# Performance work log

Hardware: AMD Instinct MI355X
Metric: run time of the kernel (lower is better)

## Reference

```python
import jax, jax.numpy as jnp
import numpy as np

B, D = 8192, 256      # batch, input_dim == n_nodes
ENC = 256             # encoder_dim
DEC = 64              # decoder_dim
THR = 0.1             # adjacency threshold


def setup_inputs() -> dict:
    key = jax.random.key(0)
    ks = jax.random.split(key, 9)
    s = lambda k, sh, fan: jax.random.normal(k, sh, jnp.float32) / np.sqrt(fan).astype(np.float32)
    return {
        "x": jax.random.normal(ks[0], (B, D), jnp.float32),
        "eps": jax.random.normal(ks[1], (B, D), jnp.float32),
        "W_enc": s(ks[2], (D, ENC), D), "b_enc": jnp.zeros((ENC,), jnp.float32),
        "W_mu": s(ks[3], (ENC, D), ENC), "b_mu": jnp.zeros((D,), jnp.float32),
        "W_lv": s(ks[4], (ENC, D), ENC), "b_lv": jnp.zeros((D,), jnp.float32),
        "graph_param": jax.random.normal(ks[5], (D, D), jnp.float32),
        "W_emb": s(ks[6], (D, DEC), 1), "b_emb": jnp.zeros((D, DEC), jnp.float32),
        "W_g1": s(ks[7], (DEC, DEC // 2), DEC), "b_g1": jnp.zeros((DEC // 2,), jnp.float32),
        "W_g2": s(ks[8], (DEC // 2, 1), DEC // 2), "b_g2": jnp.zeros((1,), jnp.float32),
        "iter_": 100,
    }


def _learned_graph(graph_param, iter_):
    # LearnedGraph.forward: sigmoid, force self-loops=1, threshold after iter 50
    g = jax.nn.sigmoid(graph_param)
    eye = jnp.eye(g.shape[0], dtype=g.dtype)
    g = g * (1.0 - eye) + eye
    if iter_ > 50:  # iter_ is a static Python int
        g = jnp.where(g > THR, g, 0.0)  # nn.Threshold(THR, 0)
    return g


def _gcn_norm(adj):
    # DGL GraphConv(norm='both') with edge_weight: messages weighted by adj values,
    # but degree normalization uses structural (unweighted) edge counts.
    mask = (adj != 0).astype(adj.dtype)
    dout = jnp.maximum(mask.sum(1), 1.0)  # out-degree of src j (row sums)
    din = jnp.maximum(mask.sum(0), 1.0)   # in-degree of dst i (col sums)
    # out[i] = sum_j adj[j,i] * x[j] / sqrt(dout[j] * din[i])  ->  M[dst, src]
    return (adj / jnp.sqrt(dout)[:, None] / jnp.sqrt(din)[None, :]).T


def reference(x, eps, W_enc, b_enc, W_mu, b_mu, W_lv, b_lv,
              graph_param, W_emb, b_emb, W_g1, b_g1, W_g2, b_g2, iter_):
    # VAE encoder (Linear + ReLU, then mu/logvar heads)
    h = jax.nn.relu(x @ W_enc + b_enc)
    mu = h @ W_mu + b_mu
    logvar = h @ W_lv + b_lv
    z = mu + eps * jnp.exp(0.5 * logvar)                 # [B, D]
    # learned adjacency over the D feature-nodes
    adj = _learned_graph(graph_param, iter_)             # [D, D]
    # per-feature node embedding: Linear(1, DEC) + tanh per feature
    b_z = jnp.tanh(z[:, :, None] * W_emb[None] + b_emb[None])  # [B, D, DEC]
    # two GraphConv layers (shared adjacency per batch element)
    M = _gcn_norm(adj)                                   # [D, D]
    h1 = jax.nn.relu(jnp.einsum('ij,bjd->bid', M, b_z) @ W_g1 + b_g1)  # [B, D, 32]
    h2 = jnp.einsum('ij,bjd->bid', M, h1) @ W_g2 + b_g2                # [B, D, 1]
    x_hat = h2.reshape(B, -1)                            # [B, D]
    return x_hat, adj, mu, logvar
```

## Files before the change

kernel.cpp:

```cpp
#include <hip/hip_runtime.h>

typedef __bf16 bf16_t;
typedef __bf16 bf16x4 __attribute__((ext_vector_type(4)));
typedef __bf16 bf16x8 __attribute__((ext_vector_type(8)));
typedef float  floatx4 __attribute__((ext_vector_type(4)));
typedef unsigned long long u64;

#define MFMA16(a, b, c) __builtin_amdgcn_mfma_f32_16x16x32_bf16((a), (b), (c), 0, 0, 0)

#define ADJ_OFF  2097152
#define MU_OFF   2162688
#define LV_OFF   4259840

#define TWO_LOG2E 2.8853900817779268f

__device__ __forceinline__ float fast_tanh2(float argE2) {
    float e = __builtin_amdgcn_exp2f(argE2);
    return 1.0f - 2.0f * __builtin_amdgcn_rcpf(e + 1.0f);
}

__device__ __forceinline__ bf16x8 cvt8(const float* p) {
    const floatx4 a = *(const floatx4*)p;
    const floatx4 b = *(const floatx4*)(p + 4);
    bf16x8 r;
#pragma unroll
    for (int j = 0; j < 4; j++) { r[j] = (bf16_t)a[j]; r[4 + j] = (bf16_t)b[j]; }
    return r;
}

__global__ __launch_bounds__(256) void k_prep(
    const float* __restrict__ We, const float* __restrict__ Wm,
    const float* __restrict__ Wl, const float* __restrict__ Wemb,
    const float* __restrict__ bemb, const float* __restrict__ gp,
    const int* __restrict__ iterp, bf16_t* __restrict__ Wt,
    bf16_t* __restrict__ wepack, bf16_t* __restrict__ bepack,
    u64* __restrict__ rowbits) {
    __shared__ float tile[32][33];
    const int b = blockIdx.x, tid = threadIdx.x;
    if (b < 192) {
        const int m = b >> 6, t6 = b & 63;
        const int K0 = (t6 >> 3) << 5, N0 = (t6 & 7) << 5;
        const float* src = (m == 0) ? We : ((m == 1) ? Wm : Wl);
#pragma unroll
        for (int p = 0; p < 4; p++) {
            const int idx = p * 256 + tid;
            tile[idx >> 5][idx & 31] = src[(K0 + (idx >> 5)) * 256 + N0 + (idx & 31)];
        }
        __syncthreads();
        bf16_t* dst = Wt + m * 65536;
#pragma unroll
        for (int p = 0; p < 4; p++) {
            const int idx = p * 256 + tid;
            const int nn = idx >> 5, kk = idx & 31;
            dst[(N0 + nn) * 256 + K0 + kk] = (bf16_t)tile[kk][nn];
        }
    } else if (b < 200) {
        const int base = (b - 192) * 2048;
#pragma unroll
        for (int p = 0; p < 8; p++) {
            const int idx = base + p * 256 + tid;
            wepack[idx] = (bf16_t)(TWO_LOG2E * Wemb[idx]);
        }
    } else if (b < 208) {
        const int base = (b - 200) * 2048;
#pragma unroll
        for (int p = 0; p < 8; p++) {
            const int idx = base + p * 256 + tid;
            bepack[idx] = (bf16_t)(TWO_LOG2E * bemb[idx]);
        }
    } else {
        const int j = b - 208;
        const bool thr = (*iterp) > 50;
        float g = 1.0f / (1.0f + expf(-gp[j * 256 + tid]));
        if (tid == j) g = 1.0f;
        if (thr && !(g > 0.1f)) g = 0.0f;
        const u64 bal = __ballot(g != 0.0f);
        if ((tid & 63) == 0) rowbits[j * 4 + (tid >> 6)] = bal;
    }
}

__global__ __launch_bounds__(256) void k_mkM(
    const float* __restrict__ gp, const int* __restrict__ iterp,
    const u64* __restrict__ rowbits, bf16_t* __restrict__ Mb,
    float* __restrict__ adjOut) {
    __shared__ u64 bits[256][4];
    const int j = blockIdx.x, t = threadIdx.x;
#pragma unroll
    for (int p = 0; p < 4; p++) {
        const int idx = p * 256 + t;
        bits[idx >> 2][idx & 3] = rowbits[idx];
    }
    __syncthreads();
    const int w64 = t >> 6, sh = t & 63;
    int cnt = 0;
#pragma unroll 8
    for (int jp = 0; jp < 256; jp++)
        cnt += (int)((bits[jp][w64] >> sh) & 1ull);
    const int rc = (int)(__popcll(bits[j][0]) + __popcll(bits[j][1]) +
                         __popcll(bits[j][2]) + __popcll(bits[j][3]));
    const float rso = rsqrtf((float)(rc < 1 ? 1 : rc));
    const float rsi = rsqrtf((float)(cnt < 1 ? 1 : cnt));
    float g = 1.0f / (1.0f + expf(-gp[j * 256 + t]));
    if (t == j) g = 1.0f;
    if ((*iterp) > 50 && !(g > 0.1f)) g = 0.0f;
    if (adjOut) adjOut[j * 256 + t] = g;
    Mb[t * 256 + j] = (bf16_t)(g * rso * rsi);
}

__global__ __launch_bounds__(512) void k_ench(
    const float* __restrict__ X, const bf16_t* __restrict__ Wt,
    const float* __restrict__ benc, const float* __restrict__ bmu,
    const float* __restrict__ blv,
    float* __restrict__ MuOut, float* __restrict__ LvOut) {
    __shared__ __align__(16) bf16_t Xs[64 * 264];
    __shared__ __align__(16) bf16_t Hs[64 * 264];
    const bf16_t* Bte = Wt;
    const bf16_t* Btm = Wt + 65536;
    const bf16_t* Btl = Wt + 131072;
    const int tid = threadIdx.x;
    const int r0 = blockIdx.x * 64;
    const int w = tid >> 6;
    const int lane = tid & 63;
    const int n = lane & 15, q = lane >> 4;
    const int cw = w * 32;
    const floatx4 z4 = {0.f, 0.f, 0.f, 0.f};

#pragma unroll
    for (int p = 0; p < 4; p++) {
        const int e0 = (p * 512 + tid) * 8;
        const int row = e0 >> 8, col = e0 & 255;
        *(bf16x8*)(Xs + row * 264 + col) = cvt8(X + (r0 + row) * 256 + col);
    }
    __syncthreads();

    floatx4 ah[4][2];
#pragma unroll
    for (int rt = 0; rt < 4; rt++)
#pragma unroll
        for (int tc = 0; tc < 2; tc++) ah[rt][tc] = z4;
#pragma unroll 2
    for (int k0 = 0; k0 < 256; k0 += 32) {
        bf16x8 a[4], b[2];
#pragma unroll
        for (int rt = 0; rt < 4; rt++)
            a[rt] = *(const bf16x8*)(Xs + (rt * 16 + n) * 264 + k0 + q * 8);
#pragma unroll
        for (int tc = 0; tc < 2; tc++)
            b[tc] = *(const bf16x8*)(Bte + (cw + tc * 16 + n) * 256 + k0 + q * 8);
#pragma unroll
        for (int rt = 0; rt < 4; rt++)
#pragma unroll
            for (int tc = 0; tc < 2; tc++)
                ah[rt][tc] = MFMA16(a[rt], b[tc], ah[rt][tc]);
    }
#pragma unroll
    for (int tc = 0; tc < 2; tc++) {
        const int col = cw + tc * 16 + n;
        const float bv = benc[col];
#pragma unroll
        for (int rt = 0; rt < 4; rt++)
#pragma unroll
            for (int r = 0; r < 4; r++)
                Hs[(rt * 16 + q * 4 + r) * 264 + col] =
                    (bf16_t)fmaxf(ah[rt][tc][r] + bv, 0.0f);
    }
    __syncthreads();

    {
        floatx4 am[4][2];
#pragma unroll
        for (int rt = 0; rt < 4; rt++)
#pragma unroll
            for (int tc = 0; tc < 2; tc++) am[rt][tc] = z4;
#pragma unroll 2
        for (int k0 = 0; k0 < 256; k0 += 32) {
            bf16x8 a[4], bm_[2];
#pragma unroll
            for (int rt = 0; rt < 4; rt++)
                a[rt] = *(const bf16x8*)(Hs + (rt * 16 + n) * 264 + k0 + q * 8);
#pragma unroll
            for (int tc = 0; tc < 2; tc++)
                bm_[tc] = *(const bf16x8*)(Btm + (cw + tc * 16 + n) * 256 + k0 + q * 8);
#pragma unroll
            for (int rt = 0; rt < 4; rt++)
#pragma unroll
                for (int tc = 0; tc < 2; tc++)
                    am[rt][tc] = MFMA16(a[rt], bm_[tc], am[rt][tc]);
        }
#pragma unroll
        for (int tc = 0; tc < 2; tc++) {
            const int col = cw + tc * 16 + n;
            const float bmv = bmu[col];
#pragma unroll
            for (int rt = 0; rt < 4; rt++)
#pragma unroll
                for (int r = 0; r < 4; r++)
                    MuOut[(r0 + rt * 16 + q * 4 + r) * 256 + col] = am[rt][tc][r] + bmv;
        }
    }

    {
        floatx4 al[4][2];
#pragma unroll
        for (int rt = 0; rt < 4; rt++)
#pragma unroll
            for (int tc = 0; tc < 2; tc++) al[rt][tc] = z4;
#pragma unroll 2
        for (int k0 = 0; k0 < 256; k0 += 32) {
            bf16x8 a[4], bl_[2];
#pragma unroll
            for (int rt = 0; rt < 4; rt++)
                a[rt] = *(const bf16x8*)(Hs + (rt * 16 + n) * 264 + k0 + q * 8);
#pragma unroll
            for (int tc = 0; tc < 2; tc++)
                bl_[tc] = *(const bf16x8*)(Btl + (cw + tc * 16 + n) * 256 + k0 + q * 8);
#pragma unroll
            for (int rt = 0; rt < 4; rt++)
#pragma unroll
                for (int tc = 0; tc < 2; tc++)
                    al[rt][tc] = MFMA16(a[rt], bl_[tc], al[rt][tc]);
        }
#pragma unroll
        for (int tc = 0; tc < 2; tc++) {
            const int col = cw + tc * 16 + n;
            const float blvv = blv[col];
#pragma unroll
            for (int rt = 0; rt < 4; rt++)
#pragma unroll
                for (int r = 0; r < 4; r++)
                    LvOut[(r0 + rt * 16 + q * 4 + r) * 256 + col] = al[rt][tc][r] + blvv;
        }
    }
}

__global__ __launch_bounds__(512, 4) void k_gcn(
    const float* __restrict__ Mu, const float* __restrict__ Lv,
    const float* __restrict__ Eps, const bf16_t* __restrict__ wepack,
    const bf16_t* __restrict__ bepack, const float* __restrict__ Wg1,
    const float* __restrict__ bg1, const float* __restrict__ Wg2,
    const bf16_t* __restrict__ Mb, float* __restrict__ Vout) {
    __shared__ __align__(16) bf16_t smem[128 * 256];
    __shared__ float zs[1024];
    const int tid = threadIdx.x;
    const int lane = tid & 63;
    const int w = tid >> 6;
    const int n = lane & 15, q = lane >> 4;
    const int bg = blockIdx.x;
    const floatx4 z4 = {0.f, 0.f, 0.f, 0.f};

    {
        const int gi = bg * 1024 + tid;
        zs[tid] = fmaf(Eps[gi], __expf(0.5f * Lv[gi]), Mu[gi]);
        const int gi2 = gi + 512;
        zs[tid + 512] = fmaf(Eps[gi2], __expf(0.5f * Lv[gi2]), Mu[gi2]);
    }

    bf16x8 wg1f[2][2];
#pragma unroll
    for (int ks = 0; ks < 2; ks++)
#pragma unroll
        for (int te = 0; te < 2; te++)
#pragma unroll
            for (int j = 0; j < 8; j++)
                wg1f[ks][te][j] = (bf16_t)Wg1[(ks * 32 + q * 8 + j) * 32 + te * 16 + n];
    __syncthreads();

#pragma unroll
    for (int jt2 = 0; jt2 < 2; jt2++) {
        const int j0 = (w * 2 + jt2) * 16;
        const int jA = j0 + n;
        const bf16x8 we0 = *(const bf16x8*)(wepack + jA * 64 + q * 8);
        const bf16x8 we1 = *(const bf16x8*)(wepack + jA * 64 + 32 + q * 8);
        const bf16x8 be0 = *(const bf16x8*)(bepack + jA * 64 + q * 8);
        const bf16x8 be1 = *(const bf16x8*)(bepack + jA * 64 + 32 + q * 8);
        float wf0[8], wf1[8], bf0[8], bf1[8];
#pragma unroll
        for (int j = 0; j < 8; j++) {
            wf0[j] = (float)we0[j]; wf1[j] = (float)we1[j];
            bf0[j] = (float)be0[j]; bf1[j] = (float)be1[j];
        }
        const int j8a = (j0 >> 3) + (q >> 1);
        const int jlo = (q & 1) * 4;
        const int sw = ((j8a ^ (n & 7)) << 3) + jlo;
#pragma unroll
        for (int bl = 0; bl < 4; bl++) {
            const float zv = zs[bl * 256 + jA];
            bf16x8 a0, a1;
#pragma unroll
            for (int j = 0; j < 8; j++) {
                a0[j] = (bf16_t)fast_tanh2(fmaf(zv, wf0[j], bf0[j]));
                a1[j] = (bf16_t)fast_tanh2(fmaf(zv, wf1[j], bf1[j]));
            }
            floatx4 c0 = z4, c1 = z4;
            c0 = MFMA16(a0, wg1f[0][0], c0);
            c0 = MFMA16(a1, wg1f[1][0], c0);
            c1 = MFMA16(a0, wg1f[0][1], c1);
            c1 = MFMA16(a1, wg1f[1][1], c1);
            bf16x4 s0, s1;
#pragma unroll
            for (int r = 0; r < 4; r++) { s0[r] = (bf16_t)c0[r]; s1[r] = (bf16_t)c1[r]; }
            *(bf16x4*)(smem + (bl * 32 + n) * 256 + sw) = s0;
            *(bf16x4*)(smem + (bl * 32 + 16 + n) * 256 + sw) = s1;
        }
    }
    __syncthreads();

    const int i0 = w * 32;
    floatx4 acc[2][8];
#pragma unroll
    for (int ti = 0; ti < 2; ti++)
#pragma unroll
        for (int tc = 0; tc < 8; tc++) acc[ti][tc] = z4;
#pragma unroll
    for (int k0 = 0; k0 < 256; k0 += 32) {
        const int k8 = k0 >> 3;
        bf16x8 a[2], b[8];
#pragma unroll
        for (int ti = 0; ti < 2; ti++)
            a[ti] = *(const bf16x8*)(Mb + (i0 + ti * 16 + n) * 256 + k0 + q * 8);
#pragma unroll
        for (int tc = 0; tc < 8; tc++)
            b[tc] = *(const bf16x8*)(smem + (tc * 16 + n) * 256 +
                                     (((k8 + q) ^ (n & 7)) << 3));
        __builtin_amdgcn_s_setprio(1);
#pragma unroll
        for (int ti = 0; ti < 2; ti++)
#pragma unroll
            for (int tc = 0; tc < 8; tc++)
                acc[ti][tc] = MFMA16(a[ti], b[tc], acc[ti][tc]);
        __builtin_amdgcn_s_setprio(0);
    }

    const float w2a = Wg2[n],      w2b = Wg2[16 + n];
    const float b1a = bg1[n],      b1b = bg1[16 + n];
    float v32[32];
#pragma unroll
    for (int bl = 0; bl < 4; bl++)
#pragma unroll
        for (int ti = 0; ti < 2; ti++)
#pragma unroll
            for (int r = 0; r < 4; r++)
                v32[bl * 8 + ti * 4 + r] =
                    fmaxf(acc[ti][2 * bl][r] + b1a, 0.0f) * w2a +
                    fmaxf(acc[ti][2 * bl + 1][r] + b1b, 0.0f) * w2b;
    const bool h0 = (lane & 1), h1_ = (lane & 2), h2 = (lane & 4), h3 = (lane & 8);
    float u16[16];
#pragma unroll
    for (int p = 0; p < 16; p++) {
        const float keep = h0 ? v32[2 * p + 1] : v32[2 * p];
        const float send = h0 ? v32[2 * p] : v32[2 * p + 1];
        u16[p] = keep + __shfl_xor(send, 1, 64);
    }
    float u8[8];
#pragma unroll
    for (int p = 0; p < 8; p++) {
        const float keep = h1_ ? u16[2 * p + 1] : u16[2 * p];
        const float send = h1_ ? u16[2 * p] : u16[2 * p + 1];
        u8[p] = keep + __shfl_xor(send, 2, 64);
    }
    float u4[4];
#pragma unroll
    for (int p = 0; p < 4; p++) {
        const float keep = h2 ? u8[2 * p + 1] : u8[2 * p];
        const float send = h2 ? u8[2 * p] : u8[2 * p + 1];
        u4[p] = keep + __shfl_xor(send, 4, 64);
    }
    float u2[2];
#pragma unroll
    for (int p = 0; p < 2; p++) {
        const float keep = h3 ? u4[2 * p + 1] : u4[2 * p];
        const float send = h3 ? u4[2 * p] : u4[2 * p + 1];
        u2[p] = keep + __shfl_xor(send, 8, 64);
    }
    {
        const int i_out = i0 + ((n >> 2) & 1) * 16 + q * 4 + (n & 3);
        const int blv = n >> 3;
        Vout[bg * 1024 + blv * 256 + i_out] = u2[0];
        Vout[bg * 1024 + (2 + blv) * 256 + i_out] = u2[1];
    }
}

__global__ __launch_bounds__(512) void k_out(
    float* __restrict__ VX, const bf16_t* __restrict__ Mb,
    const float* __restrict__ bg2) {
    __shared__ __align__(16) bf16_t va[64 * 264];
    const int tid = threadIdx.x;
    const int lane = tid & 63;
    const int w = tid >> 6;
    const int n = lane & 15, q = lane >> 4;
    const int r0 = blockIdx.x * 64;

#pragma unroll
    for (int p = 0; p < 8; p++) {
        const int i4 = p * 512 + tid;
        const int row = i4 >> 6, c4 = (i4 & 63) * 4;
        const floatx4 v = *(const floatx4*)(VX + (r0 + row) * 256 + c4);
        bf16x4 s;
#pragma unroll
        for (int r = 0; r < 4; r++) s[r] = (bf16_t)v[r];
        *(bf16x4*)(va + row * 264 + c4) = s;
    }
    __syncthreads();

    const int cw = w * 32;
    const floatx4 z4 = {0.f, 0.f, 0.f, 0.f};
    floatx4 acc[4][2];
#pragma unroll
    for (int rt = 0; rt < 4; rt++)
#pragma unroll
        for (int tc = 0; tc < 2; tc++) acc[rt][tc] = z4;
#pragma unroll 2
    for (int k0 = 0; k0 < 256; k0 += 32) {
        bf16x8 a[4], b[2];
#pragma unroll
        for (int rt = 0; rt < 4; rt++)
            a[rt] = *(const bf16x8*)(va + (rt * 16 + n) * 264 + k0 + q * 8);
#pragma unroll
        for (int tc = 0; tc < 2; tc++)
            b[tc] = *(const bf16x8*)(Mb + (cw + tc * 16 + n) * 256 + k0 + q * 8);
#pragma unroll
        for (int rt = 0; rt < 4; rt++)
#pragma unroll
            for (int tc = 0; tc < 2; tc++)
                acc[rt][tc] = MFMA16(a[rt], b[tc], acc[rt][tc]);
    }
    const float bv = bg2[0];
#pragma unroll
    for (int tc = 0; tc < 2; tc++) {
        const int col = cw + tc * 16 + n;
#pragma unroll
        for (int rt = 0; rt < 4; rt++)
#pragma unroll
            for (int r = 0; r < 4; r++)
                VX[(r0 + rt * 16 + q * 4 + r) * 256 + col] = acc[rt][tc][r] + bv;
    }
}

__global__ __launch_bounds__(256) void k_adj(
    const float* __restrict__ gp, const int* __restrict__ iterp,
    float* __restrict__ adjOut) {
    const int o = blockIdx.x * 256 + threadIdx.x;
    const int j = o >> 8, i = o & 255;
    float g = 1.0f / (1.0f + expf(-gp[o]));
    if (i == j) g = 1.0f;
    if ((*iterp) > 50 && !(g > 0.1f)) g = 0.0f;
    adjOut[o] = g;
}

extern "C" void kernel_launch(void* const* d_in, const int* in_sizes, int n_in,
                              void* d_out, int out_size, void* d_ws, size_t ws_size,
                              hipStream_t stream) {
    const float* x    = (const float*)d_in[0];
    const float* eps  = (const float*)d_in[1];
    const float* Wenc = (const float*)d_in[2];
    const float* benc = (const float*)d_in[3];
    const float* Wmu  = (const float*)d_in[4];
    const float* bmu  = (const float*)d_in[5];
    const float* Wlv  = (const float*)d_in[6];
    const float* blv  = (const float*)d_in[7];
    const float* gp   = (const float*)d_in[8];
    const float* Wemb = (const float*)d_in[9];
    const float* bemb = (const float*)d_in[10];
    const float* Wg1  = (const float*)d_in[11];
    const float* bg1  = (const float*)d_in[12];
    const float* Wg2  = (const float*)d_in[13];
    const float* bg2  = (const float*)d_in[14];
    const int*   itr  = (const int*)d_in[15];
    (void)in_sizes; (void)n_in; (void)out_size;

    float* xhat = (float*)d_out;
    float* adjO = xhat + ADJ_OFF;
    float* muo  = xhat + MU_OFF;
    float* lvo  = xhat + LV_OFF;

    const bool usews = (d_ws != nullptr && ws_size >= 262144);
    char* scr = usews ? (char*)d_ws : (char*)adjO;
    bf16_t* Mb      = (bf16_t*)scr;
    bf16_t* wepack  = (bf16_t*)(scr + 131072);
    bf16_t* bepack  = (bf16_t*)(scr + 163840);
    u64*    rowbits = (u64*)(scr + 196608);
    bf16_t* Wt      = (bf16_t*)((char*)d_out + 4194304);

    k_prep<<<dim3(464), dim3(256), 0, stream>>>(Wenc, Wmu, Wlv, Wemb, bemb,
                                                gp, itr, Wt, wepack, bepack,
                                                rowbits);
    k_mkM <<<dim3(256), dim3(256), 0, stream>>>(gp, itr, rowbits, Mb,
                                                usews ? adjO : nullptr);
    k_ench<<<dim3(128), dim3(512), 0, stream>>>(x, Wt, benc, bmu, blv, muo, lvo);
    k_gcn <<<dim3(2048), dim3(512), 0, stream>>>(muo, lvo, eps, wepack, bepack,
                                                 Wg1, bg1, Wg2, Mb, xhat);
    k_out <<<dim3(128), dim3(512), 0, stream>>>(xhat, Mb, bg2);
    if (!usews)
        k_adj<<<dim3(256), dim3(256), 0, stream>>>(gp, itr, adjO);
}
```

Before: 190.9 us.

## Merge M-build into encoder kernel, prepack Wg1, halve GCN shared tile

The normalized-adjacency builder (k_mkM) is folded into the encoder kernel as extra blocks, so one launch is removed and the two independent jobs can overlap. Wg1 is converted to bf16 once in the prep kernel, which replaces a per-block strided fp32 gather in k_gcn with vector loads. k_gcn now handles the four batch rows in two halves using a 32KB instead of 64KB shared tile and fewer accumulators. This should lower LDS and register pressure and raise occupancy, at the cost of an extra barrier and of reloading the embedding weights per half.

New measurement: 221.9 us. 16.3% more time.

```diff
diff --git a/kernel.cpp b/kernel.cpp
--- a/kernel.cpp
+++ b/kernel.cpp
@@ -32,9 +32,10 @@
     const float* __restrict__ We, const float* __restrict__ Wm,
     const float* __restrict__ Wl, const float* __restrict__ Wemb,
     const float* __restrict__ bemb, const float* __restrict__ gp,
-    const int* __restrict__ iterp, bf16_t* __restrict__ Wt,
-    bf16_t* __restrict__ wepack, bf16_t* __restrict__ bepack,
-    u64* __restrict__ rowbits) {
+    const int* __restrict__ iterp, const float* __restrict__ Wg1,
+    bf16_t* __restrict__ Wt, bf16_t* __restrict__ wepack,
+    bf16_t* __restrict__ bepack, u64* __restrict__ rowbits,
+    bf16_t* __restrict__ wg1pk) {
     __shared__ float tile[32][33];
     const int b = blockIdx.x, tid = threadIdx.x;
     if (b < 192) {
@@ -68,7 +69,7 @@
             const int idx = base + p * 256 + tid;
             bepack[idx] = (bf16_t)(TWO_LOG2E * bemb[idx]);
         }
-    } else {
+    } else if (b < 464) {
         const int j = b - 208;
         const bool thr = (*iterp) > 50;
         float g = 1.0f / (1.0f + expf(-gp[j * 256 + tid]));
@@ -76,48 +77,58 @@
         if (thr && !(g > 0.1f)) g = 0.0f;
         const u64 bal = __ballot(g != 0.0f);
         if ((tid & 63) == 0) rowbits[j * 4 + (tid >> 6)] = bal;
-    }
-}
-
-__global__ __launch_bounds__(256) void k_mkM(
-    const float* __restrict__ gp, const int* __restrict__ iterp,
-    const u64* __restrict__ rowbits, bf16_t* __restrict__ Mb,
-    float* __restrict__ adjOut) {
-    __shared__ u64 bits[256][4];
-    const int j = blockIdx.x, t = threadIdx.x;
-#pragma unroll
-    for (int p = 0; p < 4; p++) {
-        const int idx = p * 256 + t;
-        bits[idx >> 2][idx & 3] = rowbits[idx];
-    }
-    __syncthreads();
-    const int w64 = t >> 6, sh = t & 63;
-    int cnt = 0;
-#pragma unroll 8
-    for (int jp = 0; jp < 256; jp++)
-        cnt += (int)((bits[jp][w64] >> sh) & 1ull);
-    const int rc = (int)(__popcll(bits[j][0]) + __popcll(bits[j][1]) +
-                         __popcll(bits[j][2]) + __popcll(bits[j][3]));
-    const float rso = rsqrtf((float)(rc < 1 ? 1 : rc));
-    const float rsi = rsqrtf((float)(cnt < 1 ? 1 : cnt));
-    float g = 1.0f / (1.0f + expf(-gp[j * 256 + t]));
-    if (t == j) g = 1.0f;
-    if ((*iterp) > 50 && !(g > 0.1f)) g = 0.0f;
-    if (adjOut) adjOut[j * 256 + t] = g;
-    Mb[t * 256 + j] = (bf16_t)(g * rso * rsi);
-}
-
-__global__ __launch_bounds__(512) void k_ench(
+    } else {
+#pragma unroll
+        for (int idx = tid; idx < 2048; idx += 256) {
+            const int jj = idx & 7, qq = (idx >> 3) & 3, nn = (idx >> 5) & 15;
+            const int te = (idx >> 9) & 1, ks = (idx >> 10) & 1;
+            wg1pk[idx] = (bf16_t)Wg1[(ks * 32 + qq * 8 + jj) * 32 + te * 16 + nn];
+        }
+    }
+}
+
+__global__ __launch_bounds__(512) void k_mid(
     const float* __restrict__ X, const bf16_t* __restrict__ Wt,
     const float* __restrict__ benc, const float* __restrict__ bmu,
-    const float* __restrict__ blv,
-    float* __restrict__ MuOut, float* __restrict__ LvOut) {
+    const float* __restrict__ blv, float* __restrict__ MuOut,
+    float* __restrict__ LvOut, const float* __restrict__ gp,
+    const int* __restrict__ iterp, const u64* __restrict__ rowbits,
+    bf16_t* __restrict__ Mb, float* __restrict__ adjOut) {
     __shared__ __align__(16) bf16_t Xs[64 * 264];
     __shared__ __align__(16) bf16_t Hs[64 * 264];
+    const int tid = threadIdx.x;
+
+    if (blockIdx.x >= 128) {
+        u64* bits = (u64*)Xs;
+        const int jb = (blockIdx.x - 128) * 2;
+#pragma unroll
+        for (int p = 0; p < 2; p++) {
+            const int idx = p * 512 + tid;
+            bits[idx] = rowbits[idx];
+        }
+        __syncthreads();
+        const int sub = tid >> 8, col = tid & 255;
+        const int j = jb + sub;
+        const int w64 = col >> 6, sh = col & 63;
+        int cnt = 0;
+#pragma unroll 8
+        for (int jp = 0; jp < 256; jp++)
+            cnt += (int)((bits[jp * 4 + w64] >> sh) & 1ull);
+        const int rc = (int)(__popcll(bits[j * 4 + 0]) + __popcll(bits[j * 4 + 1]) +
+                             __popcll(bits[j * 4 + 2]) + __popcll(bits[j * 4 + 3]));
+        const float rso = rsqrtf((float)(rc < 1 ? 1 : rc));
+        const float rsi = rsqrtf((float)(cnt < 1 ? 1 : cnt));
+        float g = 1.0f / (1.0f + expf(-gp[j * 256 + col]));
+        if (col == j) g = 1.0f;
+        if ((*iterp) > 50 && !(g > 0.1f)) g = 0.0f;
+        if (adjOut) adjOut[j * 256 + col] = g;
+        Mb[col * 256 + j] = (bf16_t)(g * rso * rsi);
+        return;
+    }
+
     const bf16_t* Bte = Wt;
     const bf16_t* Btm = Wt + 65536;
     const bf16_t* Btl = Wt + 131072;
-    const int tid = threadIdx.x;
     const int r0 = blockIdx.x * 64;
     const int w = tid >> 6;
     const int lane = tid & 63;
@@ -236,10 +247,10 @@
 __global__ __launch_bounds__(512, 4) void k_gcn(
     const float* __restrict__ Mu, const float* __restrict__ Lv,
     const float* __restrict__ Eps, const bf16_t* __restrict__ wepack,
-    const bf16_t* __restrict__ bepack, const float* __restrict__ Wg1,
+    const bf16_t* __restrict__ bepack, const bf16_t* __restrict__ wg1pk,
     const float* __restrict__ bg1, const float* __restrict__ Wg2,
     const bf16_t* __restrict__ Mb, float* __restrict__ Vout) {
-    __shared__ __align__(16) bf16_t smem[128 * 256];
+    __shared__ __align__(16) bf16_t smem[64 * 256];
     __shared__ float zs[1024];
     const int tid = threadIdx.x;
     const int lane = tid & 63;
@@ -254,129 +265,123 @@
         const int gi2 = gi + 512;
         zs[tid + 512] = fmaf(Eps[gi2], __expf(0.5f * Lv[gi2]), Mu[gi2]);
     }
-
-    bf16x8 wg1f[2][2];
-#pragma unroll
-    for (int ks = 0; ks < 2; ks++)
-#pragma unroll
-        for (int te = 0; te < 2; te++)
-#pragma unroll
-            for (int j = 0; j < 8; j++)
-                wg1f[ks][te][j] = (bf16_t)Wg1[(ks * 32 + q * 8 + j) * 32 + te * 16 + n];
     __syncthreads();
 
-#pragma unroll
-    for (int jt2 = 0; jt2 < 2; jt2++) {
-        const int j0 = (w * 2 + jt2) * 16;
-        const int jA = j0 + n;
-        const bf16x8 we0 = *(const bf16x8*)(wepack + jA * 64 + q * 8);
-        const bf16x8 we1 = *(const bf16x8*)(wepack + jA * 64 + 32 + q * 8);
-        const bf16x8 be0 = *(const bf16x8*)(bepack + jA * 64 + q * 8);
-        const bf16x8 be1 = *(const bf16x8*)(bepack + jA * 64 + 32 + q * 8);
-        float wf0[8], wf1[8], bf0[8], bf1[8];
-#pragma unroll
-        for (int j = 0; j < 8; j++) {
-            wf0[j] = (float)we0[j]; wf1[j] = (float)we1[j];
-            bf0[j] = (float)be0[j]; bf1[j] = (float)be1[j];
-        }
-        const int j8a = (j0 >> 3) + (q >> 1);
-        const int jlo = (q & 1) * 4;
-        const int sw = ((j8a ^ (n & 7)) << 3) + jlo;
-#pragma unroll
-        for (int bl = 0; bl < 4; bl++) {
-            const float zv = zs[bl * 256 + jA];
-            bf16x8 a0, a1;
-#pragma unroll
-            for (int j = 0; j < 8; j++) {
-                a0[j] = (bf16_t)fast_tanh2(fmaf(zv, wf0[j], bf0[j]));
-                a1[j] = (bf16_t)fast_tanh2(fmaf(zv, wf1[j], bf1[j]));
+    const float w2a = Wg2[n],  w2b = Wg2[16 + n];
+    const float b1a = bg1[n],  b1b = bg1[16 + n];
+    const int i0 = w * 32;
+    const bool h0 = (lane & 1), h1_ = (lane & 2), h2 = (lane & 4), h3 = (lane & 8);
+
+#pragma unroll
+    for (int half = 0; half < 2; half++) {
+        bf16x8 wg1f[2][2];
+#pragma unroll
+        for (int ks = 0; ks < 2; ks++)
+#pragma unroll
+            for (int te = 0; te < 2; te++)
+                wg1f[ks][te] = *(const bf16x8*)(wg1pk +
+                    ((ks * 2 + te) * 16 + n) * 32 + q * 8);
+
+#pragma unroll
+        for (int jt2 = 0; jt2 < 2; jt2++) {
+            const int j0 = (w * 2 + jt2) * 16;
+            const int jA = j0 + n;
+            const bf16x8 we0 = *(const bf16x8*)(wepack + jA * 64 + q * 8);
+            const bf16x8 we1 = *(const bf16x8*)(wepack + jA * 64 + 32 + q * 8);
+            const bf16x8 be0 = *(const bf16x8*)(bepack + jA * 64 + q * 8);
+            const bf16x8 be1 = *(const bf16x8*)(bepack + jA * 64 + 32 + q * 8);
+            const int j8a = (j0 >> 3) + (q >> 1);
+            const int jlo = (q & 1) * 4;
+            const int sw = ((j8a ^ (n & 7)) << 3) + jlo;
+#pragma unroll
+            for (int blh = 0; blh < 2; blh++) {
+                const float zv = zs[(half * 2 + blh) * 256 + jA];
+                bf16x8 a0, a1;
+#pragma unroll
+                for (int j = 0; j < 8; j++) {
+                    a0[j] = (bf16_t)fast_tanh2(fmaf(zv, (float)we0[j], (float)be0[j]));
+                    a1[j] = (bf16_t)fast_tanh2(fmaf(zv, (float)we1[j], (float)be1[j]));
+                }
+                floatx4 c0 = z4, c1 = z4;
+                c0 = MFMA16(a0, wg1f[0][0], c0);
+                c0 = MFMA16(a1, wg1f[1][0], c0);
+                c1 = MFMA16(a0, wg1f[0][1], c1);
+                c1 = MFMA16(a1, wg1f[1][1], c1);
+                bf16x4 s0, s1;
+#pragma unroll
+                for (int r = 0; r < 4; r++) { s0[r] = (bf16_t)c0[r]; s1[r] = (bf16_t)c1[r]; }
+                *(bf16x4*)(smem + (blh * 32 + n) * 256 + sw) = s0;
+                *(bf16x4*)(smem + (blh * 32 + 16 + n) * 256 + sw) = s1;
             }
-            floatx4 c0 = z4, c1 = z4;
-            c0 = MFMA16(a0, wg1f[0][0], c0);
-            c0 = MFMA16(a1, wg1f[1][0], c0);
-            c1 = MFMA16(a0, wg1f[0][1], c1);
-            c1 = MFMA16(a1, wg1f[1][1], c1);
-            bf16x4 s0, s1;
-#pragma unroll
-            for (int r = 0; r < 4; r++) { s0[r] = (bf16_t)c0[r]; s1[r] = (bf16_t)c1[r]; }
-            *(bf16x4*)(smem + (bl * 32 + n) * 256 + sw) = s0;
-            *(bf16x4*)(smem + (bl * 32 + 16 + n) * 256 + sw) = s1;
-        }
-    }
-    __syncthreads();
-
-    const int i0 = w * 32;
-    floatx4 acc[2][8];
-#pragma unroll
-    for (int ti = 0; ti < 2; ti++)
-#pragma unroll
-        for (int tc = 0; tc < 8; tc++) acc[ti][tc] = z4;
-#pragma unroll
-    for (int k0 = 0; k0 < 256; k0 += 32) {
-        const int k8 = k0 >> 3;
-        bf16x8 a[2], b[8];
+        }
+        __syncthreads();
+
+        floatx4 acc[2][4];
 #pragma unroll
         for (int ti = 0; ti < 2; ti++)
-            a[ti] = *(const bf16x8*)(Mb + (i0 + ti * 16 + n) * 256 + k0 + q * 8);
-#pragma unroll
-        for (int tc = 0; tc < 8; tc++)
-            b[tc] = *(const bf16x8*)(smem + (tc * 16 + n) * 256 +
-                                     (((k8 + q) ^ (n & 7)) << 3));
-        __builtin_amdgcn_s_setprio(1);
+#pragma unroll
+            for (int tc = 0; tc < 4; tc++) acc[ti][tc] = z4;
+#pragma unroll
+        for (int k0 = 0; k0 < 256; k0 += 32) {
+            const int k8 = k0 >> 3;
+            bf16x8 a[2], b[4];
+#pragma unroll
+            for (int ti = 0; ti < 2; ti++)
+                a[ti] = *(const bf16x8*)(Mb + (i0 + ti * 16 + n) * 256 + k0 + q * 8);
+#pragma unroll
+            for (int tc = 0; tc < 4; tc++)
+                b[tc] = *(const bf16x8*)(smem + (tc * 16 + n) * 256 +
+                                         (((k8 + q) ^ (n & 7)) << 3));
+            __builtin_amdgcn_s_setprio(1);
+#pragma unroll
+            for (int ti = 0; ti < 2; ti++)
+#pragma unroll
+                for (int tc = 0; tc < 4; tc++)
+                    acc[ti][tc] = MFMA16(a[ti], b[tc], acc[ti][tc]);
+            __builtin_amdgcn_s_setprio(0);
+        }
+
+        float v16[16];
 #pragma unroll
         for (int ti = 0; ti < 2; ti++)
 #pragma unroll
-            for (int tc = 0; tc < 8; tc++)
-                acc[ti][tc] = MFMA16(a[ti], b[tc], acc[ti][tc]);
-        __builtin_amdgcn_s_setprio(0);
-    }
-
-    const float w2a = Wg2[n],      w2b = Wg2[16 + n];
-    const float b1a = bg1[n],      b1b = bg1[16 + n];
-    float v32[32];
-#pragma unroll
-    for (int bl = 0; bl < 4; bl++)
-#pragma unroll
-        for (int ti = 0; ti < 2; ti++)
-#pragma unroll
-            for (int r = 0; r < 4; r++)
-                v32[bl * 8 + ti * 4 + r] =
-                    fmaxf(acc[ti][2 * bl][r] + b1a, 0.0f) * w2a +
-                    fmaxf(acc[ti][2 * bl + 1][r] + b1b, 0.0f) * w2b;
-    const bool h0 = (lane & 1), h1_ = (lane & 2), h2 = (lane & 4), h3 = (lane & 8);
-    float u16[16];
-#pragma unroll
-    for (int p = 0; p < 16; p++) {
-        const float keep = h0 ? v32[2 * p + 1] : v32[2 * p];
-        const float send = h0 ? v32[2 * p] : v32[2 * p + 1];
-        u16[p] = keep + __shfl_xor(send, 1, 64);
-    }
-    float u8[8];
-#pragma unroll
-    for (int p = 0; p < 8; p++) {
-        const float keep = h1_ ? u16[2 * p + 1] : u16[2 * p];
-        const float send = h1_ ? u16[2 * p] : u16[2 * p + 1];
-        u8[p] = keep + __shfl_xor(send, 2, 64);
-    }
-    float u4[4];
-#pragma unroll
-    for (int p = 0; p < 4; p++) {
-        const float keep = h2 ? u8[2 * p + 1] : u8[2 * p];
-        const float send = h2 ? u8[2 * p] : u8[2 * p + 1];
-        u4[p] = keep + __shfl_xor(send, 4, 64);
-    }
-    float u2[2];
-#pragma unroll
-    for (int p = 0; p < 2; p++) {
-        const float keep = h3 ? u4[2 * p + 1] : u4[2 * p];
-        const float send = h3 ? u4[2 * p] : u4[2 * p + 1];
-        u2[p] = keep + __shfl_xor(send, 8, 64);
-    }
-    {
-        const int i_out = i0 + ((n >> 2) & 1) * 16 + q * 4 + (n & 3);
-        const int blv = n >> 3;
-        Vout[bg * 1024 + blv * 256 + i_out] = u2[0];
-        Vout[bg * 1024 + (2 + blv) * 256 + i_out] = u2[1];
+            for (int r = 0; r < 4; r++) {
+                v16[ti * 4 + r] =
+                    fmaxf(acc[ti][0][r] + b1a, 0.0f) * w2a +
+                    fmaxf(acc[ti][1][r] + b1b, 0.0f) * w2b;
+                v16[8 + ti * 4 + r] =
+                    fmaxf(acc[ti][2][r] + b1a, 0.0f) * w2a +
+                    fmaxf(acc[ti][3][r] + b1b, 0.0f) * w2b;
+            }
+        float v8[8];
+#pragma unroll
+        for (int p = 0; p < 8; p++) {
+            const float keep = h0 ? v16[2 * p + 1] : v16[2 * p];
+            const float send = h0 ? v16[2 * p] : v16[2 * p + 1];
+            v8[p] = keep + __shfl_xor(send, 1, 64);
+        }
+        float v4_[4];
+#pragma unroll
+        for (int p = 0; p < 4; p++) {
+            const float keep = h1_ ? v8[2 * p + 1] : v8[2 * p];
+            const float send = h1_ ? v8[2 * p] : v8[2 * p + 1];
+            v4_[p] = keep + __shfl_xor(send, 2, 64);
+        }
+        float v2_[2];
+#pragma unroll
+        for (int p = 0; p < 2; p++) {
+            const float keep = h2 ? v4_[2 * p + 1] : v4_[2 * p];
+            const float send = h2 ? v4_[2 * p] : v4_[2 * p + 1];
+            v2_[p] = keep + __shfl_xor(send, 4, 64);
+        }
+        {
+            const float keep = h3 ? v2_[1] : v2_[0];
+            const float send = h3 ? v2_[0] : v2_[1];
+            const float vfin = keep + __shfl_xor(send, 8, 64);
+            const int i_out = i0 + ((n >> 2) & 1) * 16 + q * 4 + (n & 3);
+            Vout[bg * 1024 + (half * 2 + (n >> 3)) * 256 + i_out] = vfin;
+        }
+        if (half == 0) __syncthreads();
     }
 }
 
@@ -479,16 +484,17 @@
     bf16_t* wepack  = (bf16_t*)(scr + 131072);
     bf16_t* bepack  = (bf16_t*)(scr + 163840);
     u64*    rowbits = (u64*)(scr + 196608);
+    bf16_t* wg1pk   = (bf16_t*)(scr + 204800);
     bf16_t* Wt      = (bf16_t*)((char*)d_out + 4194304);
 
-    k_prep<<<dim3(464), dim3(256), 0, stream>>>(Wenc, Wmu, Wlv, Wemb, bemb,
-                                                gp, itr, Wt, wepack, bepack,
-                                                rowbits);
-    k_mkM <<<dim3(256), dim3(256), 0, stream>>>(gp, itr, rowbits, Mb,
+    k_prep<<<dim3(465), dim3(256), 0, stream>>>(Wenc, Wmu, Wlv, Wemb, bemb,
+                                                gp, itr, Wg1, Wt, wepack,
+                                                bepack, rowbits, wg1pk);
+    k_mid <<<dim3(256), dim3(512), 0, stream>>>(x, Wt, benc, bmu, blv, muo,
+                                                lvo, gp, itr, rowbits, Mb,
                                                 usews ? adjO : nullptr);
-    k_ench<<<dim3(128), dim3(512), 0, stream>>>(x, Wt, benc, bmu, blv, muo, lvo);
     k_gcn <<<dim3(2048), dim3(512), 0, stream>>>(muo, lvo, eps, wepack, bepack,
-                                                 Wg1, bg1, Wg2, Mb, xhat);
+                                                 wg1pk, bg1, Wg2, Mb, xhat);
     k_out <<<dim3(128), dim3(512), 0, stream>>>(xhat, Mb, bg2);
     if (!usews)
         k_adj<<<dim3(256), dim3(256), 0, stream>>>(gp, itr, adjO);
```
